# Performance work log

Hardware: AMD Instinct MI355X
Metric: run time of the kernel (lower is better)

## Reference

```python
import jax, jax.numpy as jnp
import numpy as np

M_GROUP = 8  # VENOM m: pattern period along in_features

def _nm_mask(in_features, dtype):
    # NMVectorSparsifier.get_random_mask keeps positions 0 and 2 of every group of m=8
    pat = jnp.array([1.0, 0.0, 1.0, 0.0, 0.0, 0.0, 0.0, 0.0], dtype=dtype)
    return jnp.tile(pat, in_features // M_GROUP)  # [in_features]


def setup_inputs() -> dict:
    key = jax.random.key(0)
    k1, k2, k3 = jax.random.split(key, 3)
    B, S, D_IN, D_OUT = 8, 2048, 4096, 4096
    x = jax.random.normal(k1, (B, S, D_IN), dtype=jnp.float32)
    weight = jax.random.normal(k2, (D_OUT, D_IN), dtype=jnp.float32) * 0.02
    bias = jax.random.normal(k3, (D_OUT,), dtype=jnp.float32) * 0.02
    return {"x": x, "weight": weight, "bias": bias}


def reference(x, weight, bias):
    # y = x @ (W * mask)^T + b  -- N:M (2:8) vector-sparse linear, dense-math reference
    mask = _nm_mask(weight.shape[1], weight.dtype)  # [D_IN]
    w = weight * mask[None, :]                      # [D_OUT, D_IN]
    return jnp.einsum('bsd,od->bso', x, w) + bias
```

## Files before the change

kernel.cpp:

```cpp
#include <hip/hip_runtime.h>
#include <hip/hip_bf16.h>
#include <stdint.h>

#define MROWS 16384
#define DIN   4096
#define DOUT  4096
#define KEFF  1024

typedef __attribute__((ext_vector_type(8))) __bf16 bf16x8;
typedef __attribute__((ext_vector_type(4))) float f32x4;

__device__ __forceinline__ uint32_t f2bf_rne(float f) {
  union { float f; uint32_t u; } v; v.f = f;
  uint32_t u = v.u;
  return (u + 0x7fffu + ((u >> 16) & 1u)) >> 16;
}

__global__ void venom_gather(const float* __restrict__ src,
                             uint32_t* __restrict__ dst, int ngroups) {
  int stride = gridDim.x * blockDim.x;
  for (int i = blockIdx.x * blockDim.x + threadIdx.x; i < ngroups; i += stride) {
    const float4 v = *reinterpret_cast<const float4*>(src + (size_t)i * 8);
    uint32_t lo = f2bf_rne(v.x);
    uint32_t hi = f2bf_rne(v.z);
    dst[i] = lo | (hi << 16);
  }
}

#define BM 128
#define BN 128
#define BK 32

__global__ __launch_bounds__(256) void venom_gemm(
    const __bf16* __restrict__ A, const __bf16* __restrict__ Bm,
    const float* __restrict__ bias, float* __restrict__ C) {
  __shared__ __bf16 As[BM * BK];
  __shared__ __bf16 Bs[BN * BK];

  const int nblkN = DOUT / BN;
  int nwg = gridDim.x;
  int cpx = nwg >> 3;
  int bid = blockIdx.x;
  int swz = (bid & 7) * cpx + (bid >> 3);
  int mblk = swz / nblkN;
  int nblk = swz % nblkN;

  int t = threadIdx.x;
  int w = t >> 6;
  int l = t & 63;
  int wr = w >> 1, wc = w & 1;
  int lr = l & 15;
  int lk = (l >> 4) * 8;

  const __bf16* Ag = A + (size_t)mblk * BM * KEFF;
  const __bf16* Bg = Bm + (size_t)nblk * BN * KEFF;

  f32x4 acc[4][4] = {};

  for (int k0 = 0; k0 < KEFF; k0 += BK) {
    #pragma unroll
    for (int i = 0; i < 2; ++i) {
      int e = i * 256 + t;
      int r = e >> 2;
      int c = (e & 3) * 8;
      __builtin_amdgcn_global_load_lds(
          (const __attribute__((address_space(1))) uint32_t*)(Ag + (size_t)r * KEFF + k0 + c),
          (__attribute__((address_space(3))) uint32_t*)(&As[e * 8]), 16, 0, 0);
      __builtin_amdgcn_global_load_lds(
          (const __attribute__((address_space(1))) uint32_t*)(Bg + (size_t)r * KEFF + k0 + c),
          (__attribute__((address_space(3))) uint32_t*)(&Bs[e * 8]), 16, 0, 0);
    }
    __syncthreads();

    bf16x8 af[4], bfr[4];
    #pragma unroll
    for (int mi = 0; mi < 4; ++mi)
      af[mi] = *reinterpret_cast<const bf16x8*>(&As[(wr * 64 + mi * 16 + lr) * BK + lk]);
    #pragma unroll
    for (int ni = 0; ni < 4; ++ni)
      bfr[ni] = *reinterpret_cast<const bf16x8*>(&Bs[(wc * 64 + ni * 16 + lr) * BK + lk]);

    #pragma unroll
    for (int mi = 0; mi < 4; ++mi)
      #pragma unroll
      for (int ni = 0; ni < 4; ++ni)
        acc[mi][ni] = __builtin_amdgcn_mfma_f32_16x16x32_bf16(af[mi], bfr[ni],
                                                              acc[mi][ni], 0, 0, 0);
    __syncthreads();
  }

  int colbase = nblk * BN + wc * 64;
  int rowbase = mblk * BM + wr * 64;
  #pragma unroll
  for (int ni = 0; ni < 4; ++ni) {
    int col = colbase + ni * 16 + lr;
    float bv = bias[col];
    #pragma unroll
    for (int mi = 0; mi < 4; ++mi) {
      int row0 = rowbase + mi * 16 + (l >> 4) * 4;
      f32x4 cv = acc[mi][ni];
      #pragma unroll
      for (int j = 0; j < 4; ++j)
        C[(size_t)(row0 + j) * DOUT + col] = cv[j] + bv;
    }
  }
}

__global__ void venom_naive(const float* __restrict__ x, const float* __restrict__ w,
                            const float* __restrict__ bias, float* __restrict__ out) {
  size_t total = (size_t)MROWS * DOUT;
  size_t stride = (size_t)gridDim.x * blockDim.x;
  for (size_t idx = (size_t)blockIdx.x * blockDim.x + threadIdx.x; idx < total;
       idx += stride) {
    int m = (int)(idx / DOUT), n = (int)(idx % DOUT);
    const float* xr = x + (size_t)m * DIN;
    const float* wr = w + (size_t)n * DIN;
    float s = 0.f;
    for (int g = 0; g < DIN / 8; ++g)
      s += xr[g * 8] * wr[g * 8] + xr[g * 8 + 2] * wr[g * 8 + 2];
    out[idx] = s + bias[n];
  }
}

extern "C" void kernel_launch(void* const* d_in, const int* in_sizes, int n_in,
                              void* d_out, int out_size, void* d_ws, size_t ws_size,
                              hipStream_t stream) {
  const float* x    = (const float*)d_in[0];
  const float* wgt  = (const float*)d_in[1];
  const float* bias = (const float*)d_in[2];
  float* out = (float*)d_out;

  const size_t xg_bytes = (size_t)MROWS * KEFF * 2;
  const size_t wg_bytes = (size_t)DOUT * KEFF * 2;

  if (ws_size < xg_bytes + wg_bytes) {
    venom_naive<<<2048, 256, 0, stream>>>(x, wgt, bias, out);
    return;
  }

  uint32_t* xg = (uint32_t*)d_ws;
  uint32_t* wg = (uint32_t*)((char*)d_ws + xg_bytes);

  venom_gather<<<2048, 256, 0, stream>>>(x, xg, MROWS * (DIN / 8));
  venom_gather<<<512, 256, 0, stream>>>(wgt, wg, DOUT * (DIN / 8));

  venom_gemm<<<(MROWS / BM) * (DOUT / BN), 256, 0, stream>>>(
      (const __bf16*)xg, (const __bf16*)wg, bias, out);
}
```

Measured before the change: 302.7 us.

## Double-buffer GEMM with larger 256x256x64 tiles, LDS swizzle, and 8 waves

The bf16 MFMA GEMM moves from a 128x128x32 single-buffered tile with 4 waves to a 256x256x64 tile with 8 waves. LDS is double-buffered so the next K-tile is prefetched via global_load_lds while the current one is being multiplied, and an XOR swizzle on the LDS layout is meant to reduce bank conflicts. The aim is to raise data reuse per tile and hide global-load latency behind MFMA work, and s_setprio is used to favour the MFMA phase. In exchange, LDS use rises to 128KB per block and more registers are needed per thread, which limits occupancy. The grid also shrinks to 1024 blocks, which may leave compute units unevenly loaded on the last wave.

```diff
diff --git a/kernel.cpp b/kernel.cpp
--- a/kernel.cpp
+++ b/kernel.cpp
@@ -21,21 +21,20 @@
   int stride = gridDim.x * blockDim.x;
   for (int i = blockIdx.x * blockDim.x + threadIdx.x; i < ngroups; i += stride) {
     const float4 v = *reinterpret_cast<const float4*>(src + (size_t)i * 8);
-    uint32_t lo = f2bf_rne(v.x);
-    uint32_t hi = f2bf_rne(v.z);
-    dst[i] = lo | (hi << 16);
+    dst[i] = f2bf_rne(v.x) | (f2bf_rne(v.z) << 16);
   }
 }
 
-#define BM 128
-#define BN 128
-#define BK 32
+#define BM 256
+#define BN 256
+#define BK 64
+#define NT (KEFF / BK)
 
-__global__ __launch_bounds__(256) void venom_gemm(
+__global__ __launch_bounds__(512, 2) void venom_gemm(
     const __bf16* __restrict__ A, const __bf16* __restrict__ Bm,
     const float* __restrict__ bias, float* __restrict__ C) {
-  __shared__ __bf16 As[BM * BK];
-  __shared__ __bf16 Bs[BN * BK];
+  __shared__ __bf16 As[2][BM * BK];
+  __shared__ __bf16 Bs[2][BN * BK];
 
   const int nblkN = DOUT / BN;
   int nwg = gridDim.x;
@@ -46,64 +45,100 @@
   int nblk = swz % nblkN;
 
   int t = threadIdx.x;
-  int w = t >> 6;
-  int l = t & 63;
-  int wr = w >> 1, wc = w & 1;
-  int lr = l & 15;
-  int lk = (l >> 4) * 8;
+  int wid = t >> 6, l = t & 63;
+  int wr = wid >> 2, wc = wid & 3;
+  int lr = l & 15, lg = l >> 4;
+  int lswz = (l & 7) << 4;
 
-  const __bf16* Ag = A + (size_t)mblk * BM * KEFF;
-  const __bf16* Bg = Bm + (size_t)nblk * BN * KEFF;
+  const __bf16* Ag = A + (size_t)(mblk * BM) * KEFF;
+  const __bf16* Bg = Bm + (size_t)(nblk * BN) * KEFF;
 
-  f32x4 acc[4][4] = {};
+  f32x4 acc[8][4] = {};
 
-  for (int k0 = 0; k0 < KEFF; k0 += BK) {
+  auto stage = [&](int buf, int kt) {
+    const int k0 = kt * BK;
     #pragma unroll
-    for (int i = 0; i < 2; ++i) {
-      int e = i * 256 + t;
-      int r = e >> 2;
-      int c = (e & 3) * 8;
+    for (int i = 0; i < 4; ++i) {
+      int e = i * 512 + t;
+      int row = e >> 3;
+      int inL = ((e & 7) * 16) ^ ((row & 7) << 4);
       __builtin_amdgcn_global_load_lds(
-          (const __attribute__((address_space(1))) uint32_t*)(Ag + (size_t)r * KEFF + k0 + c),
-          (__attribute__((address_space(3))) uint32_t*)(&As[e * 8]), 16, 0, 0);
+          (const __attribute__((address_space(1))) uint32_t*)(Ag + (size_t)row * KEFF + k0 + (inL >> 1)),
+          ((__attribute__((address_space(3))) uint32_t*)&As[buf][0]) + e * 4, 16, 0, 0);
+    }
+    #pragma unroll
+    for (int i = 0; i < 4; ++i) {
+      int e = i * 512 + t;
+      int row = e >> 3;
+      int inL = ((e & 7) * 16) ^ ((row & 7) << 4);
       __builtin_amdgcn_global_load_lds(
-          (const __attribute__((address_space(1))) uint32_t*)(Bg + (size_t)r * KEFF + k0 + c),
-          (__attribute__((address_space(3))) uint32_t*)(&Bs[e * 8]), 16, 0, 0);
+          (const __attribute__((address_space(1))) uint32_t*)(Bg + (size_t)row * KEFF + k0 + (inL >> 1)),
+          ((__attribute__((address_space(3))) uint32_t*)&Bs[buf][0]) + e * 4, 16, 0, 0);
     }
-    __syncthreads();
+  };
 
-    bf16x8 af[4], bfr[4];
-    #pragma unroll
-    for (int mi = 0; mi < 4; ++mi)
-      af[mi] = *reinterpret_cast<const bf16x8*>(&As[(wr * 64 + mi * 16 + lr) * BK + lk]);
-    #pragma unroll
-    for (int ni = 0; ni < 4; ++ni)
-      bfr[ni] = *reinterpret_cast<const bf16x8*>(&Bs[(wc * 64 + ni * 16 + lr) * BK + lk]);
+  stage(0, 0);
+  asm volatile("s_waitcnt vmcnt(0)" ::: "memory");
+  __builtin_amdgcn_s_barrier();
+
+  bf16x8 bfrag[4];
+
+  for (int kt = 0; kt < NT; ++kt) {
+    int cur = kt & 1, nxt = cur ^ 1, t1 = kt + 1;
+    const char* asBase = (const char*)&As[cur][0];
+    const char* bsBase = (const char*)&Bs[cur][0];
 
     #pragma unroll
-    for (int mi = 0; mi < 4; ++mi)
+    for (int ph = 0; ph < 4; ++ph) {
+      const int mh = ph & 1, kh = ph >> 1;
+      const int kswz = (kh * 64 + lg * 16) ^ lswz;
+
+      bf16x8 af[4];
       #pragma unroll
-      for (int ni = 0; ni < 4; ++ni)
-        acc[mi][ni] = __builtin_amdgcn_mfma_f32_16x16x32_bf16(af[mi], bfr[ni],
-                                                              acc[mi][ni], 0, 0, 0);
-    __syncthreads();
+      for (int mi = 0; mi < 4; ++mi)
+        af[mi] = *(const bf16x8*)(asBase +
+                   (wr * 128 + mh * 64 + mi * 16 + lr) * 128 + kswz);
+      if (mh == 0) {
+        #pragma unroll
+        for (int ni = 0; ni < 4; ++ni)
+          bfrag[ni] = *(const bf16x8*)(bsBase +
+                       (wc * 64 + ni * 16 + lr) * 128 + kswz);
+      }
+      if (ph == 0 && t1 < NT) stage(nxt, t1);
+
+      __builtin_amdgcn_s_barrier();
+      __builtin_amdgcn_s_setprio(1);
+      #pragma unroll
+      for (int mi = 0; mi < 4; ++mi)
+        #pragma unroll
+        for (int ni = 0; ni < 4; ++ni)
+          acc[mh * 4 + mi][ni] = __builtin_amdgcn_mfma_f32_16x16x32_bf16(
+              af[mi], bfrag[ni], acc[mh * 4 + mi][ni], 0, 0, 0);
+      __builtin_amdgcn_s_setprio(0);
+      if (ph < 3) __builtin_amdgcn_s_barrier();
+    }
+
+    if (t1 < NT) asm volatile("s_waitcnt vmcnt(0)" ::: "memory");
+    __builtin_amdgcn_s_barrier();
   }
 
   int colbase = nblk * BN + wc * 64;
-  int rowbase = mblk * BM + wr * 64;
+  int rowbase = mblk * BM + wr * 128;
   #pragma unroll
-  for (int ni = 0; ni < 4; ++ni) {
-    int col = colbase + ni * 16 + lr;
-    float bv = bias[col];
+  for (int mh = 0; mh < 2; ++mh)
     #pragma unroll
     for (int mi = 0; mi < 4; ++mi) {
-      int row0 = rowbase + mi * 16 + (l >> 4) * 4;
-      f32x4 cv = acc[mi][ni];
+      int row0 = rowbase + mh * 64 + mi * 16 + lg * 4;
       #pragma unroll
-      for (int j = 0; j < 4; ++j)
-        C[(size_t)(row0 + j) * DOUT + col] = cv[j] + bv;
+      for (int ni = 0; ni < 4; ++ni) {
+        int col = colbase + ni * 16 + lr;
+        float bv = bias[col];
+        f32x4 cv = acc[mh * 4 + mi][ni];
+        #pragma unroll
+        for (int j = 0; j < 4; ++j)
+          C[(size_t)(row0 + j) * DOUT + col] = cv[j] + bv;
+      }
     }
-  }
 }
 
 __global__ void venom_naive(const float* __restrict__ x, const float* __restrict__ w,
@@ -144,6 +179,6 @@
   venom_gather<<<2048, 256, 0, stream>>>(x, xg, MROWS * (DIN / 8));
   venom_gather<<<512, 256, 0, stream>>>(wgt, wg, DOUT * (DIN / 8));
 
-  venom_gemm<<<(MROWS / BM) * (DOUT / BN), 256, 0, stream>>>(
+  venom_gemm<<<(MROWS / BM) * (DOUT / BN), 512, 0, stream>>>(
       (const __bf16*)xg, (const __bf16*)wg, bias, out);
 }
```

Result: faster. 289.8 us (-4.3%).
